# Performance work log

Measured on AMD Instinct MI355X. Metric: run time of the kernel, lower is better.

Reference implementation:

```python
import jax, jax.numpy as jnp
import numpy as np

N_NODES = 20000
N_EDGES = 320000
EMB = 128


def setup_inputs() -> dict:
    key = jax.random.key(0)
    ks = jax.random.split(key, 8)
    h = jax.random.normal(ks[0], (N_NODES, EMB), dtype=jnp.float32)
    W1 = jax.random.normal(ks[1], (2 * EMB, 4 * EMB), dtype=jnp.float32) / np.sqrt(2 * EMB)
    b1 = jnp.zeros((4 * EMB,), dtype=jnp.float32)
    W2 = jax.random.normal(ks[2], (4 * EMB, 1), dtype=jnp.float32) / np.sqrt(4 * EMB)
    b2 = jnp.zeros((1,), dtype=jnp.float32)
    # logistic-noise uniforms for RelaxedBernoulli rsample, kept away from {0,1}
    u = jax.random.uniform(ks[3], (N_EDGES,), dtype=jnp.float32, minval=1e-6, maxval=1.0 - 1e-6)
    row = jax.random.randint(ks[4], (N_EDGES,), 0, N_NODES, dtype=jnp.int32)
    col = jax.random.randint(ks[5], (N_EDGES,), 0, N_NODES, dtype=jnp.int32)
    edge_mask = -jnp.ones((N_EDGES,), dtype=jnp.int32)  # torch code initializes mask to -1
    return {"h": h, "W1": W1, "b1": b1, "W2": W2, "b2": b2,
            "u": u, "row": row, "col": col, "edge_mask": edge_mask, "hierarchy": 0}


def _segment_softmax(scores, seg, num_segments):
    m = jax.ops.segment_max(scores, seg, num_segments=num_segments)
    e = jnp.exp(scores - m[seg])
    s = jax.ops.segment_sum(e, seg, num_segments=num_segments)
    return e / s[seg]


TEMPERATURE = 1.0
RATIO = 0.5  # threshold for hard bernoulli


def reference(h, W1, b1, W2, b2, u, row, col, edge_mask, hierarchy):
    # edge gather + concat: [E, 2*EMB]
    edge_rep = jnp.concatenate([h[row], h[col]], axis=-1)
    # 2-layer MLP edge scorer -> [E]
    hid = jax.nn.relu(edge_rep @ W1 + b1)
    scores = (hid @ W2 + b2).reshape(-1)
    # segment softmax over edges grouped by source node (torch: softmax(edge_score, edge_index[0]))
    probs = _segment_softmax(scores, row, N_NODES)
    # RelaxedBernoulli(temperature, probs).rsample(): sigmoid((logits + logistic)/T)
    logits = jnp.log(probs) - jnp.log1p(-probs)
    logistic = jnp.log(u) - jnp.log1p(-u)
    y = jax.nn.sigmoid((logits + logistic) / TEMPERATURE)
    y_hard = (y > RATIO).astype(y.dtype)
    y_st = jax.lax.stop_gradient(y_hard - y) + y  # straight-through
    # edge_mask[y == 1] = hierarchy + 1
    new_mask = jnp.where(y_st == 1.0, jnp.int32(hierarchy + 1), edge_mask)
    c_idx = new_mask > 0
    s_idx = new_mask == -1
    causal_w = jnp.where(c_idx, scores, 0.0)
    spu_w = jnp.where(s_idx, -scores, 0.0)
    return scores, y_st, new_mask, causal_w, spu_w
```

## Files before the change

kernel.cpp:

```cpp
#include <hip/hip_runtime.h>
#include <math.h>

#define N_NODES 20000
#define N_EDGES 320000
#define EMB 128
#define HID 512
#define PQ_STRIDE 1024
#define ROWS_PER_BLOCK 16
#define SC_CAP 2048
#define NCHUNK ((N_NODES + 1023) / 1024)

typedef float v2f __attribute__((ext_vector_type(2)));

#if defined(__has_builtin)
#if __has_builtin(__builtin_elementwise_fma)
#define V2FMA(a, b, c) __builtin_elementwise_fma((a), (b), (c))
#else
#define V2FMA(a, b, c) ((a) * (b) + (c))
#endif
#else
#define V2FMA(a, b, c) ((a) * (b) + (c))
#endif

__global__ void init_deg(int* __restrict__ deg, int* __restrict__ offs) {
    int i = blockIdx.x * 256 + threadIdx.x;
    if (i < N_NODES) deg[i] = 0;
    if (i == 0) offs[N_NODES] = N_EDGES;
}

__global__ void histogram_rows(const int* __restrict__ row, int* __restrict__ deg) {
    int e = blockIdx.x * 256 + threadIdx.x;
    if (e < N_EDGES) atomicAdd(&deg[row[e]], 1);
}

__device__ __forceinline__ int wave_incl_scan(int v, int lane) {
#pragma unroll
    for (int off = 1; off < 64; off <<= 1) {
        int t = __shfl_up(v, off, 64);
        if (lane >= off) v += t;
    }
    return v;
}

__global__ __launch_bounds__(1024) void scan_part(const int* __restrict__ deg,
                                                  int* __restrict__ part,
                                                  int* __restrict__ totals) {
    __shared__ int wsum[16];
    const int tid = threadIdx.x, lane = tid & 63, w = tid >> 6;
    const int i = blockIdx.x * 1024 + tid;
    int v = (i < N_NODES) ? deg[i] : 0;
    int incl = wave_incl_scan(v, lane);
    if (lane == 63) wsum[w] = incl;
    __syncthreads();
    if (w == 0) {
        int x = (lane < 16) ? wsum[lane] : 0;
        int xs = wave_incl_scan(x, lane);
        if (lane < 16) wsum[lane] = xs - x;
        if (lane == 15) totals[blockIdx.x] = xs;
    }
    __syncthreads();
    if (i < N_NODES) part[i] = wsum[w] + incl - v;
}

__global__ void scan_carry(const int* __restrict__ totals, int* __restrict__ carry) {
    const int lane = threadIdx.x;
    int v = (lane < NCHUNK) ? totals[lane] : 0;
    int incl = wave_incl_scan(v, lane);
    if (lane < NCHUNK) carry[lane] = incl - v;
}

__global__ __launch_bounds__(1024) void scan_apply(const int* __restrict__ part,
                                                   const int* __restrict__ carry,
                                                   int* __restrict__ cursor,
                                                   int* __restrict__ offs) {
    const int i = blockIdx.x * 1024 + threadIdx.x;
    if (i < N_NODES) {
        int o = part[i] + carry[blockIdx.x];
        cursor[i] = o;
        offs[i] = o;
    }
}

__global__ void scatter_edges(const int* __restrict__ row, const int* __restrict__ col,
                              int* __restrict__ cursor, int2* __restrict__ rc2) {
    int e = blockIdx.x * 256 + threadIdx.x;
    if (e >= N_EDGES) return;
    int r = row[e];
    int pos = atomicAdd(&cursor[r], 1);
    rc2[pos] = make_int2(e, (r << 16) | col[e]);
}

#define TM 128
#define TN 128
#define BK 8
#define NTILES (EMB / BK)

__global__ __launch_bounds__(256) void gemm_pq(
    const float* __restrict__ h, const float* __restrict__ W1,
    const float* __restrict__ b1, float* __restrict__ PQ)
{
    __shared__ float As[2][BK][TM + 4];
    __shared__ float Bs[2][BK][TN];

    const int tid = threadIdx.x;
    const int nt  = blockIdx.x;
    const int mt  = blockIdx.y;
    const int m_base = mt * TM;

    const int a_m = tid >> 1;
    const int a_k = (tid & 1) << 2;
    const int  row_a = m_base + a_m;
    const bool a_ok  = row_a < N_NODES;
    const float* __restrict__ hrow = h + (size_t)row_a * EMB + a_k;

    const int b_k = tid >> 5;
    const int b_n = (tid & 31) << 2;
    const int w_row_off = (nt < 4) ? 0 : 128;
    const int w_col     = (nt & 3) * TN + b_n;
    const float* __restrict__ wrow = W1 + (size_t)(w_row_off + b_k) * HID + w_col;

    const int ty = tid >> 4, tx = tid & 15;
    const int cm = ty << 2, cn = tx << 2;

    v2f acc[8][4] = {};

    float4 pa, pb;
    pa = make_float4(0.f, 0.f, 0.f, 0.f);
    if (a_ok) pa = *(const float4*)(hrow);
    pb = *(const float4*)(wrow);
    As[0][a_k + 0][a_m] = pa.x;
    As[0][a_k + 1][a_m] = pa.y;
    As[0][a_k + 2][a_m] = pa.z;
    As[0][a_k + 3][a_m] = pa.w;
    *(float4*)&Bs[0][b_k][b_n] = pb;
    __syncthreads();

    for (int t = 0; t < NTILES; ++t) {
        const int cur = t & 1;
        if (t + 1 < NTILES) {
            const int k0 = (t + 1) * BK;
            pa = make_float4(0.f, 0.f, 0.f, 0.f);
            if (a_ok) pa = *(const float4*)(hrow + k0);
            pb = *(const float4*)(wrow + (size_t)k0 * HID);
        }

#pragma unroll
        for (int kk = 0; kk < BK; ++kk) {
            float a[8];
            *(float4*)&a[0] = *(const float4*)&As[cur][kk][cm];
            *(float4*)&a[4] = *(const float4*)&As[cur][kk][cm + 64];
            float4 b0 = *(const float4*)&Bs[cur][kk][cn];
            float4 b1v = *(const float4*)&Bs[cur][kk][cn + 64];
            v2f bp[4] = {(v2f){b0.x, b0.y}, (v2f){b0.z, b0.w},
                         (v2f){b1v.x, b1v.y}, (v2f){b1v.z, b1v.w}};
#pragma unroll
            for (int i = 0; i < 8; ++i) {
                v2f ai = (v2f){a[i], a[i]};
#pragma unroll
                for (int j = 0; j < 4; ++j)
                    acc[i][j] = V2FMA(ai, bp[j], acc[i][j]);
            }
        }

        if (t + 1 < NTILES) {
            const int nxt = 1 - cur;
            As[nxt][a_k + 0][a_m] = pa.x;
            As[nxt][a_k + 1][a_m] = pa.y;
            As[nxt][a_k + 2][a_m] = pa.z;
            As[nxt][a_k + 3][a_m] = pa.w;
            *(float4*)&Bs[nxt][b_k][b_n] = pb;
            __syncthreads();
        }
    }

    const int col_base = nt * TN;
    v2f bias[4] = {{0.f,0.f},{0.f,0.f},{0.f,0.f},{0.f,0.f}};
    if (nt < 4) {
        float4 bv0 = *(const float4*)(b1 + col_base + cn);
        float4 bv1 = *(const float4*)(b1 + col_base + cn + 64);
        bias[0] = (v2f){bv0.x, bv0.y};
        bias[1] = (v2f){bv0.z, bv0.w};
        bias[2] = (v2f){bv1.x, bv1.y};
        bias[3] = (v2f){bv1.z, bv1.w};
    }

#pragma unroll
    for (int i = 0; i < 8; ++i) {
        const int r = m_base + cm + (i < 4 ? i : 64 + i - 4);
        if (r < N_NODES) {
            float* dst = PQ + (size_t)r * PQ_STRIDE + col_base;
            v2f c0 = acc[i][0] + bias[0], c1 = acc[i][1] + bias[1];
            v2f c2 = acc[i][2] + bias[2], c3 = acc[i][3] + bias[3];
            *(float4*)(dst + cn)      = make_float4(c0.x, c0.y, c1.x, c1.y);
            *(float4*)(dst + cn + 64) = make_float4(c2.x, c2.y, c3.x, c3.y);
        }
    }
}

__global__ __launch_bounds__(256) void fused_edge(
    const float* __restrict__ PQ,
    const float* __restrict__ W2, const float* __restrict__ b2,
    const int2* __restrict__ rc2, const int* __restrict__ offs,
    const float* __restrict__ u, const int* __restrict__ edge_mask,
    const int* __restrict__ hierarchy,
    float* __restrict__ scores, float* __restrict__ out_y,
    float* __restrict__ out_mask, float* __restrict__ out_causal,
    float* __restrict__ out_spu)
{
    __shared__ float sc_lds[SC_CAP];

    const int r0 = blockIdx.x * ROWS_PER_BLOCK;
    const int r1 = (r0 + ROWS_PER_BLOCK < N_NODES) ? r0 + ROWS_PER_BLOCK : N_NODES;
    const int e0 = offs[r0];
    const int e1 = offs[r1];
    const int tid = threadIdx.x, lane = tid & 63, w = tid >> 6;
    const int j0 = lane << 2;

    const float4 w0 = *(const float4*)(W2 + j0);
    const float4 w1 = *(const float4*)(W2 + 256 + j0);
    const float bias2 = b2[0];

    for (int i0 = e0 + (w << 1); i0 < e1; i0 += 8) {
        const int  iA   = i0;
        const bool hasB = (i0 + 1) < e1;
        const int  iB   = hasB ? i0 + 1 : i0;

        const int2 eA = rc2[iA];
        const int2 eB = rc2[iB];
        const int rA = ((unsigned)eA.y) >> 16, cA = eA.y & 0xFFFF;
        const int rB = ((unsigned)eB.y) >> 16, cB = eB.y & 0xFFFF;
        const float* __restrict__ pA = PQ + (size_t)rA * PQ_STRIDE;
        const float* __restrict__ qA = PQ + (size_t)cA * PQ_STRIDE + HID;
        const float* __restrict__ pB = PQ + (size_t)rB * PQ_STRIDE;
        const float* __restrict__ qB = PQ + (size_t)cB * PQ_STRIDE + HID;

        float4 pA0 = *(const float4*)(pA + j0);
        float4 pA1 = *(const float4*)(pA + 256 + j0);
        float4 qA0 = *(const float4*)(qA + j0);
        float4 qA1 = *(const float4*)(qA + 256 + j0);
        float4 pB0 = *(const float4*)(pB + j0);
        float4 pB1 = *(const float4*)(pB + 256 + j0);
        float4 qB0 = *(const float4*)(qB + j0);
        float4 qB1 = *(const float4*)(qB + 256 + j0);

        float sA = 0.0f, sB = 0.0f;
        sA = fmaf(fmaxf(pA0.x + qA0.x, 0.0f), w0.x, sA);
        sA = fmaf(fmaxf(pA0.y + qA0.y, 0.0f), w0.y, sA);
        sA = fmaf(fmaxf(pA0.z + qA0.z, 0.0f), w0.z, sA);
        sA = fmaf(fmaxf(pA0.w + qA0.w, 0.0f), w0.w, sA);
        sA = fmaf(fmaxf(pA1.x + qA1.x, 0.0f), w1.x, sA);
        sA = fmaf(fmaxf(pA1.y + qA1.y, 0.0f), w1.y, sA);
        sA = fmaf(fmaxf(pA1.z + qA1.z, 0.0f), w1.z, sA);
        sA = fmaf(fmaxf(pA1.w + qA1.w, 0.0f), w1.w, sA);
        sB = fmaf(fmaxf(pB0.x + qB0.x, 0.0f), w0.x, sB);
        sB = fmaf(fmaxf(pB0.y + qB0.y, 0.0f), w0.y, sB);
        sB = fmaf(fmaxf(pB0.z + qB0.z, 0.0f), w0.z, sB);
        sB = fmaf(fmaxf(pB0.w + qB0.w, 0.0f), w0.w, sB);
        sB = fmaf(fmaxf(pB1.x + qB1.x, 0.0f), w1.x, sB);
        sB = fmaf(fmaxf(pB1.y + qB1.y, 0.0f), w1.y, sB);
        sB = fmaf(fmaxf(pB1.z + qB1.z, 0.0f), w1.z, sB);
        sB = fmaf(fmaxf(pB1.w + qB1.w, 0.0f), w1.w, sB);

#pragma unroll
        for (int off = 32; off > 0; off >>= 1) {
            sA += __shfl_down(sA, off, 64);
            sB += __shfl_down(sB, off, 64);
        }

        if (lane == 0) {
            float scA = sA + bias2;
            scores[eA.x] = scA;
            int liA = iA - e0;
            if (liA < SC_CAP) sc_lds[liA] = scA;
            if (hasB) {
                float scB = sB + bias2;
                scores[eB.x] = scB;
                int liB = iB - e0;
                if (liB < SC_CAP) sc_lds[liB] = scB;
            }
        }
    }
    __syncthreads();

    const int hv = hierarchy[0];
    for (int r = r0 + w; r < r1; r += 4) {
        const int es = offs[r], ee = offs[r + 1];
        const int d = ee - es;
        if (d == 0) continue;

        float m = -INFINITY;
        for (int j = lane; j < d; j += 64) {
            int li = es - e0 + j;
            float s = (li < SC_CAP) ? sc_lds[li] : scores[rc2[es + j].x];
            m = fmaxf(m, s);
        }
#pragma unroll
        for (int off = 32; off > 0; off >>= 1)
            m = fmaxf(m, __shfl_down(m, off, 64));
        m = __shfl(m, 0, 64);

        float ssum = 0.0f;
        for (int j = lane; j < d; j += 64) {
            int li = es - e0 + j;
            float s = (li < SC_CAP) ? sc_lds[li] : scores[rc2[es + j].x];
            ssum += expf(s - m);
        }
#pragma unroll
        for (int off = 32; off > 0; off >>= 1)
            ssum += __shfl_down(ssum, off, 64);
        ssum = __shfl(ssum, 0, 64);

        for (int j = lane; j < d; j += 64) {
            int li = es - e0 + j;
            float s = (li < SC_CAP) ? sc_lds[li] : scores[rc2[es + j].x];
            float p = expf(s - m) / ssum;
            float logits = logf(p) - log1pf(-p);
            int oe = rc2[es + j].x;
            float uu = u[oe];
            float L = logf(uu) - log1pf(-uu);
            float y = 1.0f / (1.0f + expf(-(logits + L)));
            bool hard = y > 0.5f;
            int mm = hard ? (hv + 1) : edge_mask[oe];
            out_y[oe]      = hard ? 1.0f : 0.0f;
            out_mask[oe]   = (float)mm;
            out_causal[oe] = (mm > 0)   ?  s : 0.0f;
            out_spu[oe]    = (mm == -1) ? -s : 0.0f;
        }
    }
}

extern "C" void kernel_launch(void* const* d_in, const int* in_sizes, int n_in,
                              void* d_out, int out_size, void* d_ws, size_t ws_size,
                              hipStream_t stream) {
    const float* h_ptr = (const float*)d_in[0];
    const float* W1    = (const float*)d_in[1];
    const float* b1    = (const float*)d_in[2];
    const float* W2    = (const float*)d_in[3];
    const float* b2    = (const float*)d_in[4];
    const float* u     = (const float*)d_in[5];
    const int*   row   = (const int*)d_in[6];
    const int*   col   = (const int*)d_in[7];
    const int*   emask = (const int*)d_in[8];
    const int*   hier  = (const int*)d_in[9];

    float* out        = (float*)d_out;
    float* scores     = out;
    float* out_y      = out + (size_t)N_EDGES;
    float* out_mask   = out + 2 * (size_t)N_EDGES;
    float* out_causal = out + 3 * (size_t)N_EDGES;
    float* out_spu    = out + 4 * (size_t)N_EDGES;

    float* PQ     = (float*)d_ws;
    int2*  rc2    = (int2*)(PQ + (size_t)N_NODES * PQ_STRIDE);
    int*   deg    = (int*)(rc2 + N_EDGES);
    int*   cursor = deg + N_NODES;
    int*   offs   = cursor + N_NODES;
    int*   part   = offs + N_NODES + 1;
    int*   totals = part + N_NODES;
    int*   carry  = totals + NCHUNK;

    hipLaunchKernelGGL(init_deg, dim3((N_NODES + 255) / 256), dim3(256), 0, stream,
                       deg, offs);
    hipLaunchKernelGGL(histogram_rows, dim3((N_EDGES + 255) / 256), dim3(256), 0, stream,
                       row, deg);
    hipLaunchKernelGGL(scan_part, dim3(NCHUNK), dim3(1024), 0, stream, deg, part, totals);
    hipLaunchKernelGGL(scan_carry, dim3(1), dim3(64), 0, stream, totals, carry);
    hipLaunchKernelGGL(scan_apply, dim3(NCHUNK), dim3(1024), 0, stream,
                       part, carry, cursor, offs);
    hipLaunchKernelGGL(scatter_edges, dim3((N_EDGES + 255) / 256), dim3(256), 0, stream,
                       row, col, cursor, rc2);

    dim3 ggrid(PQ_STRIDE / TN, (N_NODES + TM - 1) / TM);
    hipLaunchKernelGGL(gemm_pq, ggrid, dim3(256), 0, stream, h_ptr, W1, b1, PQ);

    hipLaunchKernelGGL(fused_edge, dim3((N_NODES + ROWS_PER_BLOCK - 1) / ROWS_PER_BLOCK),
                       dim3(256), 0, stream,
                       PQ, W2, b2, rc2, offs, u, emask, hier,
                       scores, out_y, out_mask, out_causal, out_spu);
}
```

Baseline: 302.8 us.

## Fuse row histogram into GEMM launch, fold scan carry, split P/Q buffers

```diff
diff --git a/kernel.cpp b/kernel.cpp
--- a/kernel.cpp
+++ b/kernel.cpp
@@ -5,7 +5,6 @@
 #define N_EDGES 320000
 #define EMB 128
 #define HID 512
-#define PQ_STRIDE 1024
 #define ROWS_PER_BLOCK 16
 #define SC_CAP 2048
 #define NCHUNK ((N_NODES + 1023) / 1024)
@@ -28,9 +27,126 @@
     if (i == 0) offs[N_NODES] = N_EDGES;
 }
 
-__global__ void histogram_rows(const int* __restrict__ row, int* __restrict__ deg) {
-    int e = blockIdx.x * 256 + threadIdx.x;
-    if (e < N_EDGES) atomicAdd(&deg[row[e]], 1);
+#define TM 128
+#define TN 128
+#define BK 8
+#define NTILES (EMB / BK)
+#define GEMM_MT ((N_NODES + TM - 1) / TM)
+#define GEMM_BLOCKS (8 * GEMM_MT)
+#define HIST_BLOCKS ((N_EDGES + 255) / 256)
+
+__global__ __launch_bounds__(256) void gemm_hist(
+    const float* __restrict__ h, const float* __restrict__ W1,
+    const float* __restrict__ b1, float* __restrict__ P, float* __restrict__ Q,
+    const int* __restrict__ row, int* __restrict__ deg)
+{
+    const int bid = blockIdx.x;
+    const int tid = threadIdx.x;
+
+    if (bid >= GEMM_BLOCKS) {
+        const int e = (bid - GEMM_BLOCKS) * 256 + tid;
+        if (e < N_EDGES) atomicAdd(&deg[row[e]], 1);
+        return;
+    }
+
+    __shared__ float As[2][BK][TM + 4];
+    __shared__ float Bs[2][BK][TN];
+
+    const int nt = bid & 7;
+    const int mt = bid >> 3;
+    const int m_base = mt * TM;
+
+    const int a_m = tid >> 1;
+    const int a_k = (tid & 1) << 2;
+    const int  row_a = m_base + a_m;
+    const bool a_ok  = row_a < N_NODES;
+    const float* __restrict__ hrow = h + (size_t)row_a * EMB + a_k;
+
+    const int b_k = tid >> 5;
+    const int b_n = (tid & 31) << 2;
+    const int w_row_off = (nt < 4) ? 0 : 128;
+    const int w_col     = (nt & 3) * TN + b_n;
+    const float* __restrict__ wrow = W1 + (size_t)(w_row_off + b_k) * HID + w_col;
+
+    const int ty = tid >> 4, tx = tid & 15;
+    const int cm = ty << 2, cn = tx << 2;
+
+    v2f acc[8][4] = {};
+
+    float4 pa, pb;
+    pa = make_float4(0.f, 0.f, 0.f, 0.f);
+    if (a_ok) pa = *(const float4*)(hrow);
+    pb = *(const float4*)(wrow);
+    As[0][a_k + 0][a_m] = pa.x;
+    As[0][a_k + 1][a_m] = pa.y;
+    As[0][a_k + 2][a_m] = pa.z;
+    As[0][a_k + 3][a_m] = pa.w;
+    *(float4*)&Bs[0][b_k][b_n] = pb;
+    __syncthreads();
+
+    for (int t = 0; t < NTILES; ++t) {
+        const int cur = t & 1;
+        if (t + 1 < NTILES) {
+            const int k0 = (t + 1) * BK;
+            pa = make_float4(0.f, 0.f, 0.f, 0.f);
+            if (a_ok) pa = *(const float4*)(hrow + k0);
+            pb = *(const float4*)(wrow + (size_t)k0 * HID);
+        }
+
+#pragma unroll
+        for (int kk = 0; kk < BK; ++kk) {
+            float a[8];
+            *(float4*)&a[0] = *(const float4*)&As[cur][kk][cm];
+            *(float4*)&a[4] = *(const float4*)&As[cur][kk][cm + 64];
+            float4 b0 = *(const float4*)&Bs[cur][kk][cn];
+            float4 b1v = *(const float4*)&Bs[cur][kk][cn + 64];
+            v2f bp[4] = {(v2f){b0.x, b0.y}, (v2f){b0.z, b0.w},
+                         (v2f){b1v.x, b1v.y}, (v2f){b1v.z, b1v.w}};
+#pragma unroll
+            for (int i = 0; i < 8; ++i) {
+                v2f ai = (v2f){a[i], a[i]};
+#pragma unroll
+                for (int j = 0; j < 4; ++j)
+                    acc[i][j] = V2FMA(ai, bp[j], acc[i][j]);
+            }
+        }
+
+        if (t + 1 < NTILES) {
+            const int nxt = 1 - cur;
+            As[nxt][a_k + 0][a_m] = pa.x;
+            As[nxt][a_k + 1][a_m] = pa.y;
+            As[nxt][a_k + 2][a_m] = pa.z;
+            As[nxt][a_k + 3][a_m] = pa.w;
+            *(float4*)&Bs[nxt][b_k][b_n] = pb;
+            __syncthreads();
+        }
+    }
+
+    const bool  isP = (nt < 4);
+    const int   col_base = (nt & 3) * TN;
+    float* __restrict__ dstbase = isP ? P : Q;
+
+    v2f bias[4] = {{0.f,0.f},{0.f,0.f},{0.f,0.f},{0.f,0.f}};
+    if (isP) {
+        float4 bv0 = *(const float4*)(b1 + col_base + cn);
+        float4 bv1 = *(const float4*)(b1 + col_base + cn + 64);
+        bias[0] = (v2f){bv0.x, bv0.y};
+        bias[1] = (v2f){bv0.z, bv0.w};
+        bias[2] = (v2f){bv1.x, bv1.y};
+        bias[3] = (v2f){bv1.z, bv1.w};
+    }
+
+#pragma unroll
+    for (int i = 0; i < 8; ++i) {
+        const int r = m_base + cm + (i < 4 ? i : 64 + i - 4);
+        if (r < N_NODES) {
+            float* dst = dstbase + (size_t)r * HID + col_base;
+            v2f c0 = acc[i][0] + bias[0], c1 = acc[i][1] + bias[1];
+            v2f c2 = acc[i][2] + bias[2], c3 = acc[i][3] + bias[3];
+            *(float4*)(dst + cn)      = make_float4(c0.x, c0.y, c1.x, c1.y);
+            *(float4*)(dst + cn + 64) = make_float4(c2.x, c2.y, c3.x, c3.y);
+        }
+    }
 }
 
 __device__ __forceinline__ int wave_incl_scan(int v, int lane) {
@@ -62,20 +178,21 @@
     if (i < N_NODES) part[i] = wsum[w] + incl - v;
 }
 
-__global__ void scan_carry(const int* __restrict__ totals, int* __restrict__ carry) {
-    const int lane = threadIdx.x;
-    int v = (lane < NCHUNK) ? totals[lane] : 0;
-    int incl = wave_incl_scan(v, lane);
-    if (lane < NCHUNK) carry[lane] = incl - v;
-}
-
 __global__ __launch_bounds__(1024) void scan_apply(const int* __restrict__ part,
-                                                   const int* __restrict__ carry,
+                                                   const int* __restrict__ totals,
                                                    int* __restrict__ cursor,
                                                    int* __restrict__ offs) {
-    const int i = blockIdx.x * 1024 + threadIdx.x;
+    __shared__ int carry_s;
+    const int tid = threadIdx.x;
+    if (tid < 64) {
+        int v = (tid < NCHUNK) ? totals[tid] : 0;
+        int incl = wave_incl_scan(v, tid);
+        if (tid == (int)blockIdx.x) carry_s = incl - v;
+    }
+    __syncthreads();
+    const int i = blockIdx.x * 1024 + tid;
     if (i < N_NODES) {
-        int o = part[i] + carry[blockIdx.x];
+        int o = part[i] + carry_s;
         cursor[i] = o;
         offs[i] = o;
     }
@@ -90,115 +207,8 @@
     rc2[pos] = make_int2(e, (r << 16) | col[e]);
 }
 
-#define TM 128
-#define TN 128
-#define BK 8
-#define NTILES (EMB / BK)
-
-__global__ __launch_bounds__(256) void gemm_pq(
-    const float* __restrict__ h, const float* __restrict__ W1,
-    const float* __restrict__ b1, float* __restrict__ PQ)
-{
-    __shared__ float As[2][BK][TM + 4];
-    __shared__ float Bs[2][BK][TN];
-
-    const int tid = threadIdx.x;
-    const int nt  = blockIdx.x;
-    const int mt  = blockIdx.y;
-    const int m_base = mt * TM;
-
-    const int a_m = tid >> 1;
-    const int a_k = (tid & 1) << 2;
-    const int  row_a = m_base + a_m;
-    const bool a_ok  = row_a < N_NODES;
-    const float* __restrict__ hrow = h + (size_t)row_a * EMB + a_k;
-
-    const int b_k = tid >> 5;
-    const int b_n = (tid & 31) << 2;
-    const int w_row_off = (nt < 4) ? 0 : 128;
-    const int w_col     = (nt & 3) * TN + b_n;
-    const float* __restrict__ wrow = W1 + (size_t)(w_row_off + b_k) * HID + w_col;
-
-    const int ty = tid >> 4, tx = tid & 15;
-    const int cm = ty << 2, cn = tx << 2;
-
-    v2f acc[8][4] = {};
-
-    float4 pa, pb;
-    pa = make_float4(0.f, 0.f, 0.f, 0.f);
-    if (a_ok) pa = *(const float4*)(hrow);
-    pb = *(const float4*)(wrow);
-    As[0][a_k + 0][a_m] = pa.x;
-    As[0][a_k + 1][a_m] = pa.y;
-    As[0][a_k + 2][a_m] = pa.z;
-    As[0][a_k + 3][a_m] = pa.w;
-    *(float4*)&Bs[0][b_k][b_n] = pb;
-    __syncthreads();
-
-    for (int t = 0; t < NTILES; ++t) {
-        const int cur = t & 1;
-        if (t + 1 < NTILES) {
-            const int k0 = (t + 1) * BK;
-            pa = make_float4(0.f, 0.f, 0.f, 0.f);
-            if (a_ok) pa = *(const float4*)(hrow + k0);
-            pb = *(const float4*)(wrow + (size_t)k0 * HID);
-        }
-
-#pragma unroll
-        for (int kk = 0; kk < BK; ++kk) {
-            float a[8];
-            *(float4*)&a[0] = *(const float4*)&As[cur][kk][cm];
-            *(float4*)&a[4] = *(const float4*)&As[cur][kk][cm + 64];
-            float4 b0 = *(const float4*)&Bs[cur][kk][cn];
-            float4 b1v = *(const float4*)&Bs[cur][kk][cn + 64];
-            v2f bp[4] = {(v2f){b0.x, b0.y}, (v2f){b0.z, b0.w},
-                         (v2f){b1v.x, b1v.y}, (v2f){b1v.z, b1v.w}};
-#pragma unroll
-            for (int i = 0; i < 8; ++i) {
-                v2f ai = (v2f){a[i], a[i]};
-#pragma unroll
-                for (int j = 0; j < 4; ++j)
-                    acc[i][j] = V2FMA(ai, bp[j], acc[i][j]);
-            }
-        }
-
-        if (t + 1 < NTILES) {
-            const int nxt = 1 - cur;
-            As[nxt][a_k + 0][a_m] = pa.x;
-            As[nxt][a_k + 1][a_m] = pa.y;
-            As[nxt][a_k + 2][a_m] = pa.z;
-            As[nxt][a_k + 3][a_m] = pa.w;
-            *(float4*)&Bs[nxt][b_k][b_n] = pb;
-            __syncthreads();
-        }
-    }
-
-    const int col_base = nt * TN;
-    v2f bias[4] = {{0.f,0.f},{0.f,0.f},{0.f,0.f},{0.f,0.f}};
-    if (nt < 4) {
-        float4 bv0 = *(const float4*)(b1 + col_base + cn);
-        float4 bv1 = *(const float4*)(b1 + col_base + cn + 64);
-        bias[0] = (v2f){bv0.x, bv0.y};
-        bias[1] = (v2f){bv0.z, bv0.w};
-        bias[2] = (v2f){bv1.x, bv1.y};
-        bias[3] = (v2f){bv1.z, bv1.w};
-    }
-
-#pragma unroll
-    for (int i = 0; i < 8; ++i) {
-        const int r = m_base + cm + (i < 4 ? i : 64 + i - 4);
-        if (r < N_NODES) {
-            float* dst = PQ + (size_t)r * PQ_STRIDE + col_base;
-            v2f c0 = acc[i][0] + bias[0], c1 = acc[i][1] + bias[1];
-            v2f c2 = acc[i][2] + bias[2], c3 = acc[i][3] + bias[3];
-            *(float4*)(dst + cn)      = make_float4(c0.x, c0.y, c1.x, c1.y);
-            *(float4*)(dst + cn + 64) = make_float4(c2.x, c2.y, c3.x, c3.y);
-        }
-    }
-}
-
 __global__ __launch_bounds__(256) void fused_edge(
-    const float* __restrict__ PQ,
+    const float* __restrict__ P, const float* __restrict__ Q,
     const float* __restrict__ W2, const float* __restrict__ b2,
     const int2* __restrict__ rc2, const int* __restrict__ offs,
     const float* __restrict__ u, const int* __restrict__ edge_mask,
@@ -229,10 +239,10 @@
         const int2 eB = rc2[iB];
         const int rA = ((unsigned)eA.y) >> 16, cA = eA.y & 0xFFFF;
         const int rB = ((unsigned)eB.y) >> 16, cB = eB.y & 0xFFFF;
-        const float* __restrict__ pA = PQ + (size_t)rA * PQ_STRIDE;
-        const float* __restrict__ qA = PQ + (size_t)cA * PQ_STRIDE + HID;
-        const float* __restrict__ pB = PQ + (size_t)rB * PQ_STRIDE;
-        const float* __restrict__ qB = PQ + (size_t)cB * PQ_STRIDE + HID;
+        const float* __restrict__ pA = P + (size_t)rA * HID;
+        const float* __restrict__ qA = Q + (size_t)cA * HID;
+        const float* __restrict__ pB = P + (size_t)rB * HID;
+        const float* __restrict__ qB = Q + (size_t)cB * HID;
 
         float4 pA0 = *(const float4*)(pA + j0);
         float4 pA1 = *(const float4*)(pA + 256 + j0);
@@ -350,31 +360,29 @@
     float* out_causal = out + 3 * (size_t)N_EDGES;
     float* out_spu    = out + 4 * (size_t)N_EDGES;
 
-    float* PQ     = (float*)d_ws;
-    int2*  rc2    = (int2*)(PQ + (size_t)N_NODES * PQ_STRIDE);
+    float* P      = (float*)d_ws;
+    float* Qm     = P + (size_t)N_NODES * HID;
+    int2*  rc2    = (int2*)(Qm + (size_t)N_NODES * HID);
     int*   deg    = (int*)(rc2 + N_EDGES);
     int*   cursor = deg + N_NODES;
     int*   offs   = cursor + N_NODES;
     int*   part   = offs + N_NODES + 1;
     int*   totals = part + N_NODES;
-    int*   carry  = totals + NCHUNK;
 
     hipLaunchKernelGGL(init_deg, dim3((N_NODES + 255) / 256), dim3(256), 0, stream,
                        deg, offs);
-    hipLaunchKernelGGL(histogram_rows, dim3((N_EDGES + 255) / 256), dim3(256), 0, stream,
-                       row, deg);
+
+    hipLaunchKernelGGL(gemm_hist, dim3(GEMM_BLOCKS + HIST_BLOCKS), dim3(256), 0, stream,
+                       h_ptr, W1, b1, P, Qm, row, deg);
+
     hipLaunchKernelGGL(scan_part, dim3(NCHUNK), dim3(1024), 0, stream, deg, part, totals);
-    hipLaunchKernelGGL(scan_carry, dim3(1), dim3(64), 0, stream, totals, carry);
     hipLaunchKernelGGL(scan_apply, dim3(NCHUNK), dim3(1024), 0, stream,
-                       part, carry, cursor, offs);
+                       part, totals, cursor, offs);
     hipLaunchKernelGGL(scatter_edges, dim3((N_EDGES + 255) / 256), dim3(256), 0, stream,
                        row, col, cursor, rc2);
 
-    dim3 ggrid(PQ_STRIDE / TN, (N_NODES + TM - 1) / TM);
-    hipLaunchKernelGGL(gemm_pq, ggrid, dim3(256), 0, stream, h_ptr, W1, b1, PQ);
-
     hipLaunchKernelGGL(fused_edge, dim3((N_NODES + ROWS_PER_BLOCK - 1) / ROWS_PER_BLOCK),
                        dim3(256), 0, stream,
-                       PQ, W2, b2, rc2, offs, u, emask, hier,
+                       P, Qm, W2, b2, rc2, offs, u, emask, hier,
                        scores, out_y, out_mask, out_causal, out_spu);
 }
```

New measurement: 286.5 us. 5.4% less time.
